# Performance work log

Hardware: AMD Instinct MI355X
Metric: run time of the kernel (lower is better)

## Reference

```python
import jax, jax.numpy as jnp
import numpy as np

N_NODES = 100_000
N_EDGES = 1_600_000
F_NODE = 16
F_EDGE = 8
HID = 128
N_GRAPHS = 2048


def setup_inputs() -> dict:
    key = jax.random.key(0)
    ks = jax.random.split(key, 20)
    inp = {
        "node_attr": jax.random.normal(ks[0], (N_NODES, F_NODE), dtype=jnp.float32),
        "edge_attr": jax.random.normal(ks[1], (N_EDGES, F_EDGE), dtype=jnp.float32),
        "edge_index": jax.random.randint(ks[2], (2, N_EDGES), 0, N_NODES),
        "adj_index": jax.random.randint(ks[3], (2, N_EDGES), 0, N_NODES),
        "adj_value": jax.random.uniform(ks[4], (N_EDGES,), dtype=jnp.float32) * 0.1,
        "batch": jnp.sort(jax.random.randint(ks[5], (N_NODES,), 0, N_GRAPHS)),
    }
    def glorot(k, shape):
        fan_in, fan_out = shape[0], shape[1]
        std = jnp.sqrt(2.0 / (fan_in + fan_out)).astype(jnp.float32)
        return jax.random.normal(k, shape, dtype=jnp.float32) * std
    # attr embedder params
    inp["W_node"] = glorot(ks[6], (F_NODE, HID))
    inp["W_edge"] = glorot(ks[7], (F_EDGE, HID))
    inp["b_embed"] = jnp.zeros((HID,), dtype=jnp.float32)
    # 3 GCN layers
    inp["W1"] = glorot(ks[8], (HID, HID)); inp["b1"] = jnp.zeros((HID,), jnp.float32)
    inp["W2"] = glorot(ks[9], (HID, HID)); inp["b2"] = jnp.zeros((HID,), jnp.float32)
    inp["W3"] = glorot(ks[10], (HID, HID)); inp["b3"] = jnp.zeros((HID,), jnp.float32)
    # predictor MLP
    inp["Wp1"] = glorot(ks[11], (HID, HID)); inp["bp1"] = jnp.full((HID,), 0.01, jnp.float32)
    inp["Wp2"] = glorot(ks[12], (HID, 1));   inp["bp2"] = jnp.full((1,), 0.01, jnp.float32)
    return inp


def _forward(node_attr, edge_attr, adj_value,
             W_node, W_edge, b_embed, W1, b1, W2, b2, W3, b3,
             Wp1, bp1, Wp2, bp2, edge_index, adj_index, batch):
    # --- attr embedder: mix node feats with edge feats scattered to dst nodes ---
    he = edge_attr @ W_edge                                   # [E, H]
    agg = jax.ops.segment_sum(he, edge_index[1], num_segments=N_NODES)
    h = jax.nn.relu(node_attr @ W_node + agg + b_embed)       # [N, H]

    # --- GCN stack: h <- relu(tilde_A @ (h W) + b) via sparse COO SpMM ---
    src, dst = adj_index[0], adj_index[1]
    def gcn(h, W, b):
        hw = h @ W + b                                        # [N, H]
        msg = adj_value[:, None] * hw[dst]                    # [E, H] gather
        return jax.nn.relu(jax.ops.segment_sum(msg, src, num_segments=N_NODES))
    h = gcn(h, W1, b1)
    h = gcn(h, W2, b2)
    h = gcn(h, W3, b3)

    # --- global_add_pool over graphs ---
    fp = jax.ops.segment_sum(h, batch, num_segments=N_GRAPHS)  # [G, H]

    # --- predictor MLP ---
    z = jax.nn.relu(fp @ Wp1 + bp1)
    return z @ Wp2 + bp2                                       # [G, 1]


def reference(node_attr, edge_attr, edge_index, adj_index, adj_value, batch,
              W_node, W_edge, b_embed, W1, b1, W2, b2, W3, b3,
              Wp1, bp1, Wp2, bp2):
    return _forward(node_attr, edge_attr, adj_value,
                    W_node, W_edge, b_embed, W1, b1, W2, b2, W3, b3,
                    Wp1, bp1, Wp2, bp2, edge_index, adj_index, batch)
```

## Files before the change

### kernel.cpp

```cpp
#include <hip/hip_runtime.h>

#define H 128
#define FN 16
#define FE 8
#define NBUK_MAX 1600

__global__ __launch_bounds__(256) void k_hist2(
    const int* __restrict__ k1, const int* __restrict__ k2,
    int* __restrict__ bcnt1, int* __restrict__ bcnt2, int E, int nbuk) {
  __shared__ int h1[NBUK_MAX], h2[NBUK_MAX];
  for (int i = threadIdx.x; i < nbuk; i += 256) { h1[i] = 0; h2[i] = 0; }
  __syncthreads();
  for (int e = blockIdx.x * 256 + threadIdx.x; e < E; e += 512 * 256) {
    atomicAdd(&h1[k1[e] >> 6], 1);
    atomicAdd(&h2[k2[e] >> 6], 1);
  }
  __syncthreads();
  for (int i = threadIdx.x; i < nbuk; i += 256) {
    if (h1[i]) atomicAdd(&bcnt1[i], h1[i]);
    if (h2[i]) atomicAdd(&bcnt2[i], h2[i]);
  }
}

__global__ __launch_bounds__(1024) void k_scan(
    const int* __restrict__ cnt1, int* __restrict__ st1, int* __restrict__ gc1,
    const int* __restrict__ cnt2, int* __restrict__ st2, int* __restrict__ gc2,
    int nbuk) {
  __shared__ int s[1024];
  int tid = threadIdx.x;
  for (int pass = 0; pass < 2; pass++) {
    const int* cnt = pass ? cnt2 : cnt1;
    int* st = pass ? st2 : st1;
    int* gc = pass ? gc2 : gc1;
    int run = 0;
    for (int half = 0; half * 1024 < nbuk; half++) {
      int i = half * 1024 + tid;
      int v = (i < nbuk) ? cnt[i] : 0;
      s[tid] = v; __syncthreads();
      for (int off = 1; off < 1024; off <<= 1) {
        int t = (tid >= off) ? s[tid - off] : 0;
        __syncthreads();
        s[tid] += t;
        __syncthreads();
      }
      int excl = run + s[tid] - v;
      if (i < nbuk) { st[i] = excl; gc[i] = excl; }
      run += s[1023];
      __syncthreads();
    }
    if (tid == 0) st[nbuk] = run;
    __syncthreads();
  }
}

__global__ __launch_bounds__(256) void k_p1_both(
    const int* __restrict__ k1, const int* __restrict__ adj, const float* __restrict__ vals,
    int* __restrict__ gcur1, int* __restrict__ gcur2,
    int* __restrict__ pkey, int2* __restrict__ bpay, int E, int nbuk, int p1b) {
  __shared__ int hc[NBUK_MAX];
  int tid = threadIdx.x;
  bool packed = (int)blockIdx.x < p1b;
  int chunk = packed ? blockIdx.x : blockIdx.x - p1b;
  const int* key = packed ? k1 : adj;
  int* gcur = packed ? gcur1 : gcur2;
  int c0 = chunk * 8192;
  int c1 = min(c0 + 8192, E);
  for (int i = tid; i < nbuk; i += 256) hc[i] = 0;
  __syncthreads();
  for (int e = c0 + tid; e < c1; e += 256)
    atomicAdd(&hc[key[e] >> 6], 1);
  __syncthreads();
  for (int i = tid; i < nbuk; i += 256) {
    int c = hc[i];
    if (c) hc[i] = atomicAdd(&gcur[i], c);
  }
  __syncthreads();
  if (packed) {
    for (int e = c0 + tid; e < c1; e += 256) {
      int k = key[e];
      int pos = atomicAdd(&hc[k >> 6], 1);
      pkey[pos] = (e << 6) | (k & 63);
    }
  } else {
    const int* dsts = adj + E;
    for (int e = c0 + tid; e < c1; e += 256) {
      int k = key[e];
      int pos = atomicAdd(&hc[k >> 6], 1);
      bpay[pos] = make_int2(dsts[e] | ((k & 63) << 20), __float_as_int(vals[e]));
    }
  }
}

__global__ __launch_bounds__(256) void k_agg_p2(
    const int* __restrict__ pkey, const float* __restrict__ edge_attr,
    const int* __restrict__ bst1,
    const float* __restrict__ node_attr, const float* __restrict__ Wn,
    const float* __restrict__ We8, const float* __restrict__ bemb,
    float* __restrict__ hout,
    const int2* __restrict__ bpay, const int* __restrict__ bst2,
    int* __restrict__ offs, int2* __restrict__ payF, float* __restrict__ rs,
    int N, int E, int nbuk) {
  __shared__ float lds[FE][64];
  __shared__ float na[64][FN];
  __shared__ int cnt[64], scn[64], cur[64];
  __shared__ float vsum[64];
  int tid = threadIdx.x;

  if ((int)blockIdx.x < nbuk) {
    int b = blockIdx.x;
    int node0 = b * 64;
    int col = tid & 127;
    int half = tid >> 7;
    float wreg[FN + FE];
#pragma unroll
    for (int k = 0; k < FN; k++) wreg[k] = Wn[k * H + col];
#pragma unroll
    for (int k = 0; k < FE; k++) wreg[FN + k] = We8[k * H + col];
    float bcol = bemb[col];

    for (int i = tid; i < FE * 64; i += 256) ((float*)lds)[i] = 0.f;
    for (int i = tid; i < 64 * FN; i += 256) {
      int n = node0 + (i >> 4);
      na[i >> 4][i & 15] = (n < N) ? node_attr[(size_t)n * FN + (i & 15)] : 0.f;
    }
    __syncthreads();
    int s = bst1[b], t = bst1[b + 1];
    int i = s + tid;
    for (; i + 256 < t; i += 512) {
      int pk0 = pkey[i], pk1 = pkey[i + 256];
      const float4* e0 = (const float4*)(edge_attr + (size_t)(pk0 >> 6) * FE);
      const float4* e1 = (const float4*)(edge_attr + (size_t)(pk1 >> 6) * FE);
      float4 a0 = e0[0], b0 = e0[1], a1 = e1[0], b1 = e1[1];
      int s0 = pk0 & 63, s1 = pk1 & 63;
      atomicAdd(&lds[0][s0], a0.x);  atomicAdd(&lds[1][s0], a0.y);
      atomicAdd(&lds[2][s0], a0.z);  atomicAdd(&lds[3][s0], a0.w);
      atomicAdd(&lds[4][s0], b0.x);  atomicAdd(&lds[5][s0], b0.y);
      atomicAdd(&lds[6][s0], b0.z);  atomicAdd(&lds[7][s0], b0.w);
      atomicAdd(&lds[0][s1], a1.x);  atomicAdd(&lds[1][s1], a1.y);
      atomicAdd(&lds[2][s1], a1.z);  atomicAdd(&lds[3][s1], a1.w);
      atomicAdd(&lds[4][s1], b1.x);  atomicAdd(&lds[5][s1], b1.y);
      atomicAdd(&lds[6][s1], b1.z);  atomicAdd(&lds[7][s1], b1.w);
    }
    for (; i < t; i += 256) {
      int pk = pkey[i];
      int e = pk >> 6, slot = pk & 63;
      const float4* ea = (const float4*)(edge_attr + (size_t)e * FE);
      float4 a = ea[0], b4 = ea[1];
      atomicAdd(&lds[0][slot], a.x);  atomicAdd(&lds[1][slot], a.y);
      atomicAdd(&lds[2][slot], a.z);  atomicAdd(&lds[3][slot], a.w);
      atomicAdd(&lds[4][slot], b4.x); atomicAdd(&lds[5][slot], b4.y);
      atomicAdd(&lds[6][slot], b4.z); atomicAdd(&lds[7][slot], b4.w);
    }
    __syncthreads();
    for (int pr = 0; pr < 32; pr++) {
      int nl = pr * 2 + half;
      int n = node0 + nl;
      float acc = bcol;
#pragma unroll
      for (int k = 0; k < FN; k++) acc += na[nl][k] * wreg[k];
#pragma unroll
      for (int k = 0; k < FE; k++) acc += lds[k][nl] * wreg[FN + k];
      if (n < N) hout[(size_t)n * H + col] = fmaxf(acc, 0.f);
    }
  } else {
    int b = blockIdx.x - nbuk;
    int s = bst2[b], t = bst2[b + 1];
    if (tid < 64) { cnt[tid] = 0; vsum[tid] = 0.f; }
    __syncthreads();
    for (int i = s + tid; i < t; i += 256) atomicAdd(&cnt[(bpay[i].x >> 20) & 63], 1);
    __syncthreads();
    if (tid < 64) scn[tid] = cnt[tid];
    __syncthreads();
    for (int off = 1; off < 64; off <<= 1) {
      int v = 0;
      if (tid < 64 && tid >= off) v = scn[tid - off];
      __syncthreads();
      if (tid < 64 && tid >= off) scn[tid] += v;
      __syncthreads();
    }
    if (tid < 64) {
      int excl = s + scn[tid] - cnt[tid];
      cur[tid] = excl;
      int node = b * 64 + tid;
      if (node < N) offs[node] = excl;
    }
    if (b == 0 && tid == 0) offs[N] = E;
    __syncthreads();
    for (int i = s + tid; i < t; i += 256) {
      int2 p = bpay[i];
      int slot = (p.x >> 20) & 63;
      int pos = atomicAdd(&cur[slot], 1);
      payF[pos] = make_int2(p.x & 0xFFFFF, p.y);
      atomicAdd(&vsum[slot], __int_as_float(p.y));
    }
    __syncthreads();
    if (tid < 64) {
      int node = b * 64 + tid;
      if (node < N) rs[node] = vsum[tid];
    }
  }
}

__global__ __launch_bounds__(256) void k_fused(
    const float* __restrict__ h, const int* __restrict__ offs,
    const int2* __restrict__ pay, const float* __restrict__ W,
    const float* __restrict__ bias, const float* __restrict__ rs,
    float* __restrict__ out, int N) {
  __shared__ float4 hs4[64 * 32];
  int tid = threadIdx.x;
  int c  = tid & 31;
  int rg = tid >> 5;
  int base = blockIdx.x * 64;
  const float4* h4 = (const float4*)h;

  for (int r = 0; r < 8; r++) {
    int row = rg * 8 + r;
    int n = base + row;
    float4 a0 = make_float4(0.f, 0.f, 0.f, 0.f);
    float4 a1 = make_float4(0.f, 0.f, 0.f, 0.f);
    float4 a2 = make_float4(0.f, 0.f, 0.f, 0.f);
    float4 a3 = make_float4(0.f, 0.f, 0.f, 0.f);
    if (n < N) {
      int s = offs[n], t = offs[n + 1];
      int i = s, t4 = s + ((t - s) & ~3);
      for (; i < t4; i += 4) {
        int2 p0 = pay[i], p1 = pay[i + 1], p2 = pay[i + 2], p3 = pay[i + 3];
        float4 h0 = h4[(size_t)p0.x * 32 + c];
        float4 h1 = h4[(size_t)p1.x * 32 + c];
        float4 h2 = h4[(size_t)p2.x * 32 + c];
        float4 h3 = h4[(size_t)p3.x * 32 + c];
        float v0 = __int_as_float(p0.y), v1 = __int_as_float(p1.y);
        float v2 = __int_as_float(p2.y), v3 = __int_as_float(p3.y);
        a0.x += v0 * h0.x; a0.y += v0 * h0.y; a0.z += v0 * h0.z; a0.w += v0 * h0.w;
        a1.x += v1 * h1.x; a1.y += v1 * h1.y; a1.z += v1 * h1.z; a1.w += v1 * h1.w;
        a2.x += v2 * h2.x; a2.y += v2 * h2.y; a2.z += v2 * h2.z; a2.w += v2 * h2.w;
        a3.x += v3 * h3.x; a3.y += v3 * h3.y; a3.z += v3 * h3.z; a3.w += v3 * h3.w;
      }
      for (; i < t; i++) {
        int2 p = pay[i];
        float v = __int_as_float(p.y);
        float4 hv = h4[(size_t)p.x * 32 + c];
        a0.x += v * hv.x; a0.y += v * hv.y; a0.z += v * hv.z; a0.w += v * hv.w;
      }
    }
    hs4[row * 32 + c] = make_float4(a0.x + a1.x + a2.x + a3.x,
                                    a0.y + a1.y + a2.y + a3.y,
                                    a0.z + a1.z + a2.z + a3.z,
                                    a0.w + a1.w + a2.w + a3.w);
  }
  __syncthreads();

  const float4* W4 = (const float4*)W;
  float4 acc[8];
#pragma unroll
  for (int i = 0; i < 8; i++) acc[i] = make_float4(0.f, 0.f, 0.f, 0.f);
#pragma unroll 2
  for (int k = 0; k < 32; k++) {
    float4 w0 = W4[(k * 4 + 0) * 32 + c];
    float4 w1 = W4[(k * 4 + 1) * 32 + c];
    float4 w2 = W4[(k * 4 + 2) * 32 + c];
    float4 w3 = W4[(k * 4 + 3) * 32 + c];
#pragma unroll
    for (int i = 0; i < 8; i++) {
      float4 hv = hs4[(rg + 8 * i) * 32 + k];
      acc[i].x += hv.x * w0.x + hv.y * w1.x + hv.z * w2.x + hv.w * w3.x;
      acc[i].y += hv.x * w0.y + hv.y * w1.y + hv.z * w2.y + hv.w * w3.y;
      acc[i].z += hv.x * w0.z + hv.y * w1.z + hv.z * w2.z + hv.w * w3.z;
      acc[i].w += hv.x * w0.w + hv.y * w1.w + hv.z * w2.w + hv.w * w3.w;
    }
  }

  float4 bv = ((const float4*)bias)[c];
#pragma unroll
  for (int i = 0; i < 8; i++) {
    int row = rg + 8 * i;
    int n = base + row;
    if (n < N) {
      float rsv = rs[n];
      float4 o;
      o.x = fmaxf(acc[i].x + rsv * bv.x, 0.f);
      o.y = fmaxf(acc[i].y + rsv * bv.y, 0.f);
      o.z = fmaxf(acc[i].z + rsv * bv.z, 0.f);
      o.w = fmaxf(acc[i].w + rsv * bv.w, 0.f);
      ((float4*)out)[(size_t)n * 32 + c] = o;
    }
  }
}

__global__ __launch_bounds__(256) void k_fused_pool(
    const float* __restrict__ h, const int* __restrict__ offs,
    const int2* __restrict__ pay, const float* __restrict__ W,
    const float* __restrict__ bias, const float* __restrict__ rs,
    const int* __restrict__ batch, float* __restrict__ fpool, int N) {
  __shared__ float4 hs4[64 * 32];
  __shared__ float4 psum[8][32];
  __shared__ int btl[64];
  int tid = threadIdx.x;
  int c  = tid & 31;
  int rg = tid >> 5;
  int base = blockIdx.x * 64;
  const float4* h4 = (const float4*)h;
  if (tid < 64) btl[tid] = (base + tid < N) ? batch[base + tid] : -1;

  for (int r = 0; r < 8; r++) {
    int row = rg * 8 + r;
    int n = base + row;
    float4 a0 = make_float4(0.f, 0.f, 0.f, 0.f);
    float4 a1 = make_float4(0.f, 0.f, 0.f, 0.f);
    float4 a2 = make_float4(0.f, 0.f, 0.f, 0.f);
    float4 a3 = make_float4(0.f, 0.f, 0.f, 0.f);
    if (n < N) {
      int s = offs[n], t = offs[n + 1];
      int i = s, t4 = s + ((t - s) & ~3);
      for (; i < t4; i += 4) {
        int2 p0 = pay[i], p1 = pay[i + 1], p2 = pay[i + 2], p3 = pay[i + 3];
        float4 h0 = h4[(size_t)p0.x * 32 + c];
        float4 h1 = h4[(size_t)p1.x * 32 + c];
        float4 h2 = h4[(size_t)p2.x * 32 + c];
        float4 h3 = h4[(size_t)p3.x * 32 + c];
        float v0 = __int_as_float(p0.y), v1 = __int_as_float(p1.y);
        float v2 = __int_as_float(p2.y), v3 = __int_as_float(p3.y);
        a0.x += v0 * h0.x; a0.y += v0 * h0.y; a0.z += v0 * h0.z; a0.w += v0 * h0.w;
        a1.x += v1 * h1.x; a1.y += v1 * h1.y; a1.z += v1 * h1.z; a1.w += v1 * h1.w;
        a2.x += v2 * h2.x; a2.y += v2 * h2.y; a2.z += v2 * h2.z; a2.w += v2 * h2.w;
        a3.x += v3 * h3.x; a3.y += v3 * h3.y; a3.z += v3 * h3.z; a3.w += v3 * h3.w;
      }
      for (; i < t; i++) {
        int2 p = pay[i];
        float v = __int_as_float(p.y);
        float4 hv = h4[(size_t)p.x * 32 + c];
        a0.x += v * hv.x; a0.y += v * hv.y; a0.z += v * hv.z; a0.w += v * hv.w;
      }
    }
    hs4[row * 32 + c] = make_float4(a0.x + a1.x + a2.x + a3.x,
                                    a0.y + a1.y + a2.y + a3.y,
                                    a0.z + a1.z + a2.z + a3.z,
                                    a0.w + a1.w + a2.w + a3.w);
  }
  __syncthreads();

  const float4* W4 = (const float4*)W;
  float4 acc[8];
#pragma unroll
  for (int i = 0; i < 8; i++) acc[i] = make_float4(0.f, 0.f, 0.f, 0.f);
#pragma unroll 2
  for (int k = 0; k < 32; k++) {
    float4 w0 = W4[(k * 4 + 0) * 32 + c];
    float4 w1 = W4[(k * 4 + 1) * 32 + c];
    float4 w2 = W4[(k * 4 + 2) * 32 + c];
    float4 w3 = W4[(k * 4 + 3) * 32 + c];
#pragma unroll
    for (int i = 0; i < 8; i++) {
      float4 hv = hs4[(rg + 8 * i) * 32 + k];
      acc[i].x += hv.x * w0.x + hv.y * w1.x + hv.z * w2.x + hv.w * w3.x;
      acc[i].y += hv.x * w0.y + hv.y * w1.y + hv.z * w2.y + hv.w * w3.y;
      acc[i].z += hv.x * w0.z + hv.y * w1.z + hv.z * w2.z + hv.w * w3.z;
      acc[i].w += hv.x * w0.w + hv.y * w1.w + hv.z * w2.w + hv.w * w3.w;
    }
  }

  float4 bv = ((const float4*)bias)[c];
  __syncthreads();
#pragma unroll
  for (int i = 0; i < 8; i++) {
    int row = rg + 8 * i;
    int n = base + row;
    float4 o = make_float4(0.f, 0.f, 0.f, 0.f);
    if (n < N) {
      float rsv = rs[n];
      o.x = fmaxf(acc[i].x + rsv * bv.x, 0.f);
      o.y = fmaxf(acc[i].y + rsv * bv.y, 0.f);
      o.z = fmaxf(acc[i].z + rsv * bv.z, 0.f);
      o.w = fmaxf(acc[i].w + rsv * bv.w, 0.f);
    }
    hs4[row * 32 + c] = o;
  }
  __syncthreads();

  int g0 = btl[0];
  int g1 = g0;
  for (int r = 1; r < 64; r++) { int bb = btl[r]; if (bb >= 0) g1 = bb; }
  for (int gr = g0; gr <= g1; gr++) {
    float4 s = make_float4(0.f, 0.f, 0.f, 0.f);
#pragma unroll
    for (int r = rg * 8; r < rg * 8 + 8; r++) {
      if (btl[r] == gr) {
        float4 v = hs4[r * 32 + c];
        s.x += v.x; s.y += v.y; s.z += v.z; s.w += v.w;
      }
    }
    psum[rg][c] = s;
    __syncthreads();
    if (rg == 0) {
      float4 tot = psum[0][c];
#pragma unroll
      for (int j = 1; j < 8; j++) {
        float4 v = psum[j][c];
        tot.x += v.x; tot.y += v.y; tot.z += v.z; tot.w += v.w;
      }
      float* dst = fpool + (size_t)gr * H + c * 4;
      atomicAdd(dst + 0, tot.x);
      atomicAdd(dst + 1, tot.y);
      atomicAdd(dst + 2, tot.z);
      atomicAdd(dst + 3, tot.w);
    }
    __syncthreads();
  }
}

__global__ __launch_bounds__(256) void k_gemm_pred(
    const float* __restrict__ in, const float* __restrict__ W,
    const float* __restrict__ bias, const float* __restrict__ Wp2,
    const float* __restrict__ bp2, float* __restrict__ out, int N) {
  __shared__ float4 hs4[64 * 32];
  int tid = threadIdx.x;
  int c  = tid & 31;
  int rg = tid >> 5;
  int rowBase = blockIdx.x * 64;
  const float4* in4 = (const float4*)in;
  const float4* W4  = (const float4*)W;
#pragma unroll
  for (int j = 0; j < 8; j++) {
    int q = tid + 256 * j;
    int r = rowBase + (q >> 5);
    int rr = (r < N) ? r : (N - 1);
    hs4[q] = in4[(size_t)rr * 32 + (q & 31)];
  }
  __syncthreads();
  float4 acc[8];
#pragma unroll
  for (int i = 0; i < 8; i++) acc[i] = make_float4(0.f, 0.f, 0.f, 0.f);
#pragma unroll 2
  for (int k = 0; k < 32; k++) {
    float4 w0 = W4[(k * 4 + 0) * 32 + c];
    float4 w1 = W4[(k * 4 + 1) * 32 + c];
    float4 w2 = W4[(k * 4 + 2) * 32 + c];
    float4 w3 = W4[(k * 4 + 3) * 32 + c];
#pragma unroll
    for (int i = 0; i < 8; i++) {
      float4 hv = hs4[(rg + 8 * i) * 32 + k];
      acc[i].x += hv.x * w0.x + hv.y * w1.x + hv.z * w2.x + hv.w * w3.x;
      acc[i].y += hv.x * w0.y + hv.y * w1.y + hv.z * w2.y + hv.w * w3.y;
      acc[i].z += hv.x * w0.z + hv.y * w1.z + hv.z * w2.z + hv.w * w3.z;
      acc[i].w += hv.x * w0.w + hv.y * w1.w + hv.z * w2.w + hv.w * w3.w;
    }
  }
  float4 bv = ((const float4*)bias)[c];
  float4 wp = ((const float4*)Wp2)[c];
  float bp = bp2[0];
#pragma unroll
  for (int i = 0; i < 8; i++) {
    int row = rowBase + rg + 8 * i;
    float4 o;
    o.x = fmaxf(acc[i].x + bv.x, 0.f);
    o.y = fmaxf(acc[i].y + bv.y, 0.f);
    o.z = fmaxf(acc[i].z + bv.z, 0.f);
    o.w = fmaxf(acc[i].w + bv.w, 0.f);
    float v = o.x * wp.x + o.y * wp.y + o.z * wp.z + o.w * wp.w;
#pragma unroll
    for (int off = 16; off > 0; off >>= 1) v += __shfl_down(v, off, 32);
    if (c == 0 && row < N) out[row] = v + bp;
  }
}

extern "C" void kernel_launch(void* const* d_in, const int* in_sizes, int n_in,
                              void* d_out, int out_size, void* d_ws, size_t ws_size,
                              hipStream_t stream) {
  const float* node_attr  = (const float*)d_in[0];
  const float* edge_attr  = (const float*)d_in[1];
  const int*   edge_index = (const int*)d_in[2];
  const int*   adj_index  = (const int*)d_in[3];
  const float* adj_value  = (const float*)d_in[4];
  const int*   batch      = (const int*)d_in[5];
  const float* W_node  = (const float*)d_in[6];
  const float* W_edge  = (const float*)d_in[7];
  const float* b_embed = (const float*)d_in[8];
  const float* W1 = (const float*)d_in[9];
  const float* b1 = (const float*)d_in[10];
  const float* W2 = (const float*)d_in[11];
  const float* b2 = (const float*)d_in[12];
  const float* W3 = (const float*)d_in[13];
  const float* b3 = (const float*)d_in[14];
  const float* Wp1 = (const float*)d_in[15];
  const float* bp1 = (const float*)d_in[16];
  const float* Wp2 = (const float*)d_in[17];
  const float* bp2 = (const float*)d_in[18];
  float* out = (float*)d_out;

  const int E = in_sizes[4];
  const int N = in_sizes[5];
  const int G = out_size;
  const int nbuk = (N + 63) >> 6;
  const int p1b = (E + 8191) / 8192;

  float* A     = (float*)d_ws;
  float* B     = A + (size_t)N * H;
  int2*  payF  = (int2*)(B + (size_t)N * H);
  float* fpool = (float*)(payF + E);
  int*   bcnt1 = (int*)(fpool + (size_t)G * H);
  int*   bcnt2 = bcnt1 + nbuk;
  int*   bst1  = bcnt2 + nbuk;
  int*   gcur1 = bst1 + nbuk + 1;
  int*   bst2  = gcur1 + nbuk;
  int*   gcur2 = bst2 + nbuk + 1;
  int*   offs2 = gcur2 + nbuk;
  float* rs    = (float*)(offs2 + N + 1);
  int*   pkey  = (int*)B;
  int2*  bpay2 = (int2*)(((int*)B) + E);

  hipMemsetAsync(fpool, 0, (size_t)G * H * sizeof(float) + 2 * nbuk * sizeof(int), stream);
  k_hist2<<<512, 256, 0, stream>>>(edge_index + E, adj_index, bcnt1, bcnt2, E, nbuk);
  k_scan<<<1, 1024, 0, stream>>>(bcnt1, bst1, gcur1, bcnt2, bst2, gcur2, nbuk);

  k_p1_both<<<2 * p1b, 256, 0, stream>>>(edge_index + E, adj_index, adj_value,
                                         gcur1, gcur2, pkey, bpay2, E, nbuk, p1b);

  k_agg_p2<<<2 * nbuk, 256, 0, stream>>>(pkey, edge_attr, bst1,
                                         node_attr, W_node, W_edge, b_embed, A,
                                         bpay2, bst2, offs2, payF, rs, N, E, nbuk);

  int lb = (N + 63) / 64;
  k_fused<<<lb, 256, 0, stream>>>(A, offs2, payF, W1, b1, rs, B, N);
  k_fused<<<lb, 256, 0, stream>>>(B, offs2, payF, W2, b2, rs, A, N);
  k_fused_pool<<<lb, 256, 0, stream>>>(A, offs2, payF, W3, b3, rs, batch, fpool, N);

  k_gemm_pred<<<(G + 63) / 64, 256, 0, stream>>>(fpool, Wp1, bp1, Wp2, bp2, out, G);
}
```

Baseline: 856.3 us.

## Scatter edge attributes during bucketing and split embedding into separate kernel

The bucketing pass now copies each edge's 8-float attribute vector into bucket order as two float4 arrays plus a slot array, replacing the packed edge-id key. The aggregation kernel then streams these contiguously instead of doing random gathers from edge_attr. The node embedding matmul moves out of the aggregation blocks into a new grid-stride kernel that reads an 8-wide aggregate per node and the staged weights. The change also doubles the bucketing chunk size and cuts the histogram grid from 512 to 128 blocks. In exchange it writes and rereads about 36 bytes per edge, launches one extra kernel, and round-trips the small per-node aggregate through global memory.

```diff
diff --git a/kernel.cpp b/kernel.cpp
--- a/kernel.cpp
+++ b/kernel.cpp
@@ -4,6 +4,7 @@
 #define FN 16
 #define FE 8
 #define NBUK_MAX 1600
+#define P1CHUNK 16384
 
 __global__ __launch_bounds__(256) void k_hist2(
     const int* __restrict__ k1, const int* __restrict__ k2,
@@ -11,7 +12,7 @@
   __shared__ int h1[NBUK_MAX], h2[NBUK_MAX];
   for (int i = threadIdx.x; i < nbuk; i += 256) { h1[i] = 0; h2[i] = 0; }
   __syncthreads();
-  for (int e = blockIdx.x * 256 + threadIdx.x; e < E; e += 512 * 256) {
+  for (int e = blockIdx.x * 256 + threadIdx.x; e < E; e += 128 * 256) {
     atomicAdd(&h1[k1[e] >> 6], 1);
     atomicAdd(&h2[k2[e] >> 6], 1);
   }
@@ -54,17 +55,19 @@
 }
 
 __global__ __launch_bounds__(256) void k_p1_both(
-    const int* __restrict__ k1, const int* __restrict__ adj, const float* __restrict__ vals,
+    const int* __restrict__ k1, const float* __restrict__ edge_attr,
+    const int* __restrict__ adj, const float* __restrict__ vals,
     int* __restrict__ gcur1, int* __restrict__ gcur2,
-    int* __restrict__ pkey, int2* __restrict__ bpay, int E, int nbuk, int p1b) {
+    float4* __restrict__ pattrA, float4* __restrict__ pattrB, int* __restrict__ pslot,
+    int2* __restrict__ bpay, int E, int nbuk, int p1b) {
   __shared__ int hc[NBUK_MAX];
   int tid = threadIdx.x;
   bool packed = (int)blockIdx.x < p1b;
   int chunk = packed ? blockIdx.x : blockIdx.x - p1b;
   const int* key = packed ? k1 : adj;
   int* gcur = packed ? gcur1 : gcur2;
-  int c0 = chunk * 8192;
-  int c1 = min(c0 + 8192, E);
+  int c0 = chunk * P1CHUNK;
+  int c1 = min(c0 + P1CHUNK, E);
   for (int i = tid; i < nbuk; i += 256) hc[i] = 0;
   __syncthreads();
   for (int e = c0 + tid; e < c1; e += 256)
@@ -76,10 +79,13 @@
   }
   __syncthreads();
   if (packed) {
+    const float4* ea4 = (const float4*)edge_attr;
     for (int e = c0 + tid; e < c1; e += 256) {
       int k = key[e];
       int pos = atomicAdd(&hc[k >> 6], 1);
-      pkey[pos] = (e << 6) | (k & 63);
+      pattrA[pos] = ea4[(size_t)e * 2 + 0];
+      pattrB[pos] = ea4[(size_t)e * 2 + 1];
+      pslot[pos] = k & 63;
     }
   } else {
     const int* dsts = adj + E;
@@ -92,16 +98,13 @@
 }
 
 __global__ __launch_bounds__(256) void k_agg_p2(
-    const int* __restrict__ pkey, const float* __restrict__ edge_attr,
-    const int* __restrict__ bst1,
-    const float* __restrict__ node_attr, const float* __restrict__ Wn,
-    const float* __restrict__ We8, const float* __restrict__ bemb,
-    float* __restrict__ hout,
+    const float4* __restrict__ pattrA, const float4* __restrict__ pattrB,
+    const int* __restrict__ pslot, const int* __restrict__ bst1,
+    float* __restrict__ agg8,
     const int2* __restrict__ bpay, const int* __restrict__ bst2,
     int* __restrict__ offs, int2* __restrict__ payF, float* __restrict__ rs,
     int N, int E, int nbuk) {
   __shared__ float lds[FE][64];
-  __shared__ float na[64][FN];
   __shared__ int cnt[64], scn[64], cur[64];
   __shared__ float vsum[64];
   int tid = threadIdx.x;
@@ -109,29 +112,14 @@
   if ((int)blockIdx.x < nbuk) {
     int b = blockIdx.x;
     int node0 = b * 64;
-    int col = tid & 127;
-    int half = tid >> 7;
-    float wreg[FN + FE];
-#pragma unroll
-    for (int k = 0; k < FN; k++) wreg[k] = Wn[k * H + col];
-#pragma unroll
-    for (int k = 0; k < FE; k++) wreg[FN + k] = We8[k * H + col];
-    float bcol = bemb[col];
-
     for (int i = tid; i < FE * 64; i += 256) ((float*)lds)[i] = 0.f;
-    for (int i = tid; i < 64 * FN; i += 256) {
-      int n = node0 + (i >> 4);
-      na[i >> 4][i & 15] = (n < N) ? node_attr[(size_t)n * FN + (i & 15)] : 0.f;
-    }
     __syncthreads();
     int s = bst1[b], t = bst1[b + 1];
     int i = s + tid;
     for (; i + 256 < t; i += 512) {
-      int pk0 = pkey[i], pk1 = pkey[i + 256];
-      const float4* e0 = (const float4*)(edge_attr + (size_t)(pk0 >> 6) * FE);
-      const float4* e1 = (const float4*)(edge_attr + (size_t)(pk1 >> 6) * FE);
-      float4 a0 = e0[0], b0 = e0[1], a1 = e1[0], b1 = e1[1];
-      int s0 = pk0 & 63, s1 = pk1 & 63;
+      int s0 = pslot[i], s1 = pslot[i + 256];
+      float4 a0 = pattrA[i], b0 = pattrB[i];
+      float4 a1 = pattrA[i + 256], b1 = pattrB[i + 256];
       atomicAdd(&lds[0][s0], a0.x);  atomicAdd(&lds[1][s0], a0.y);
       atomicAdd(&lds[2][s0], a0.z);  atomicAdd(&lds[3][s0], a0.w);
       atomicAdd(&lds[4][s0], b0.x);  atomicAdd(&lds[5][s0], b0.y);
@@ -142,25 +130,17 @@
       atomicAdd(&lds[6][s1], b1.z);  atomicAdd(&lds[7][s1], b1.w);
     }
     for (; i < t; i += 256) {
-      int pk = pkey[i];
-      int e = pk >> 6, slot = pk & 63;
-      const float4* ea = (const float4*)(edge_attr + (size_t)e * FE);
-      float4 a = ea[0], b4 = ea[1];
+      int slot = pslot[i];
+      float4 a = pattrA[i], b4 = pattrB[i];
       atomicAdd(&lds[0][slot], a.x);  atomicAdd(&lds[1][slot], a.y);
       atomicAdd(&lds[2][slot], a.z);  atomicAdd(&lds[3][slot], a.w);
       atomicAdd(&lds[4][slot], b4.x); atomicAdd(&lds[5][slot], b4.y);
       atomicAdd(&lds[6][slot], b4.z); atomicAdd(&lds[7][slot], b4.w);
     }
     __syncthreads();
-    for (int pr = 0; pr < 32; pr++) {
-      int nl = pr * 2 + half;
-      int n = node0 + nl;
-      float acc = bcol;
-#pragma unroll
-      for (int k = 0; k < FN; k++) acc += na[nl][k] * wreg[k];
-#pragma unroll
-      for (int k = 0; k < FE; k++) acc += lds[k][nl] * wreg[FN + k];
-      if (n < N) hout[(size_t)n * H + col] = fmaxf(acc, 0.f);
+    for (int j = tid; j < 64 * FE; j += 256) {
+      int n = node0 + (j >> 3);
+      if (n < N) agg8[(size_t)n * FE + (j & 7)] = lds[j & 7][j >> 3];
     }
   } else {
     int b = blockIdx.x - nbuk;
@@ -197,6 +177,37 @@
     if (tid < 64) {
       int node = b * 64 + tid;
       if (node < N) rs[node] = vsum[tid];
+    }
+  }
+}
+
+__global__ __launch_bounds__(256) void k_embed_h(
+    const float* __restrict__ node_attr, const float* __restrict__ Wn,
+    const float* __restrict__ We8, const float* __restrict__ b,
+    const float* __restrict__ agg8, float* __restrict__ h, int N) {
+  __shared__ float Ws[FN * H];
+  __shared__ float Es[FE * H];
+  __shared__ float na[2][FN];
+  __shared__ float a8[2][FE];
+  for (int i = threadIdx.x; i < FN * H; i += 256) Ws[i] = Wn[i];
+  for (int i = threadIdx.x; i < FE * H; i += 256) Es[i] = We8[i];
+  int lane = threadIdx.x & 127;
+  int sub  = threadIdx.x >> 7;
+  for (int n0 = blockIdx.x * 2; n0 < N; n0 += gridDim.x * 2) {
+    int n = n0 + sub;
+    __syncthreads();
+    if (n < N) {
+      if (lane < FN) na[sub][lane] = node_attr[(size_t)n * FN + lane];
+      else if (lane < FN + FE) a8[sub][lane - FN] = agg8[(size_t)n * FE + (lane - FN)];
+    }
+    __syncthreads();
+    if (n < N) {
+      float acc = b[lane];
+#pragma unroll
+      for (int k = 0; k < FN; k++) acc += na[sub][k] * Ws[k * H + lane];
+#pragma unroll
+      for (int k = 0; k < FE; k++) acc += a8[sub][k] * Es[k * H + lane];
+      h[(size_t)n * H + lane] = fmaxf(acc, 0.f);
     }
   }
 }
@@ -491,7 +502,7 @@
   const int N = in_sizes[5];
   const int G = out_size;
   const int nbuk = (N + 63) >> 6;
-  const int p1b = (E + 8191) / 8192;
+  const int p1b = (E + P1CHUNK - 1) / P1CHUNK;
 
   float* A     = (float*)d_ws;
   float* B     = A + (size_t)N * H;
@@ -505,19 +516,24 @@
   int*   gcur2 = bst2 + nbuk + 1;
   int*   offs2 = gcur2 + nbuk;
   float* rs    = (float*)(offs2 + N + 1);
-  int*   pkey  = (int*)B;
-  int2*  bpay2 = (int2*)(((int*)B) + E);
+  float4* pattrA = (float4*)A;
+  float4* pattrB = pattrA + E;
+  int*    pslot  = (int*)B;
+  int2*   bpay2  = (int2*)(pslot + E);
+  float*  agg8   = (float*)(bpay2 + E);
 
   hipMemsetAsync(fpool, 0, (size_t)G * H * sizeof(float) + 2 * nbuk * sizeof(int), stream);
-  k_hist2<<<512, 256, 0, stream>>>(edge_index + E, adj_index, bcnt1, bcnt2, E, nbuk);
+  k_hist2<<<128, 256, 0, stream>>>(edge_index + E, adj_index, bcnt1, bcnt2, E, nbuk);
   k_scan<<<1, 1024, 0, stream>>>(bcnt1, bst1, gcur1, bcnt2, bst2, gcur2, nbuk);
 
-  k_p1_both<<<2 * p1b, 256, 0, stream>>>(edge_index + E, adj_index, adj_value,
-                                         gcur1, gcur2, pkey, bpay2, E, nbuk, p1b);
-
-  k_agg_p2<<<2 * nbuk, 256, 0, stream>>>(pkey, edge_attr, bst1,
-                                         node_attr, W_node, W_edge, b_embed, A,
+  k_p1_both<<<2 * p1b, 256, 0, stream>>>(edge_index + E, edge_attr, adj_index, adj_value,
+                                         gcur1, gcur2, pattrA, pattrB, pslot, bpay2,
+                                         E, nbuk, p1b);
+
+  k_agg_p2<<<2 * nbuk, 256, 0, stream>>>(pattrA, pattrB, pslot, bst1, agg8,
                                          bpay2, bst2, offs2, payF, rs, N, E, nbuk);
+
+  k_embed_h<<<4096, 256, 0, stream>>>(node_attr, W_node, W_edge, b_embed, agg8, A, N);
 
   int lb = (N + 63) / 64;
   k_fused<<<lb, 256, 0, stream>>>(A, offs2, payF, W1, b1, rs, B, N);
```

After: 1.034 ms. +20.7%, slower.
